# Kernel tuning notes

Measured on AMD Instinct MI355X. Metric: run time of the kernel, lower is better.

The kernel has to match this reference:

```python
import jax, jax.numpy as jnp
import numpy as np

NUM_LABELS = 10  # number of distinct label values in the minibatch
EPS = 1e-8


def setup_inputs() -> dict:
    key = jax.random.key(0)
    k1, k2 = jax.random.split(key)
    z = jax.random.normal(k1, (8192, 20, 256), dtype=jnp.float32)  # [B, C, H]
    labels = jax.random.randint(k2, (8192,), 0, NUM_LABELS)  # [B]
    return {"z": z, "labels": labels}


def reference(z, labels):
    # CODI minibatch loss, positive pairs, representation space.
    # Equivalent to: for each unique label, mse(z[group] + 1e-8, mean(z[group]))
    # summed over labels. Vectorized as a single segment-mean +
    # gather-broadcast + segment-SSE pass (one traversal of z).
    z = jnp.nan_to_num(z)
    B, C, H = z.shape
    counts = jax.ops.segment_sum(
        jnp.ones((B,), dtype=z.dtype), labels, num_segments=NUM_LABELS
    )  # [K]
    sums = jax.ops.segment_sum(z, labels, num_segments=NUM_LABELS)  # [K, C, H]
    means = jnp.nan_to_num(sums / jnp.maximum(counts, 1.0)[:, None, None])
    # per-sample squared distance to its group's mean (note the +EPS as in torch)
    d = (z + EPS) - means[labels]  # [B, C, H]
    per_sample = jnp.sum(d * d, axis=(1, 2))  # [B]
    sse = jax.ops.segment_sum(per_sample, labels, num_segments=NUM_LABELS)  # [K]
    # nn.MSELoss is a mean over all elements of the group: count_k * C * H
    mse_k = sse / (jnp.maximum(counts, 1.0) * (C * H))
    # torch.unique only visits labels present in the batch -> mask empty groups
    return jnp.sum(jnp.where(counts > 0, jnp.nan_to_num(mse_k), 0.0))
```

## Files before the change

### kernel.cpp

```cpp
#include <hip/hip_runtime.h>

#define B_SZ   8192
#define CH     5120
#define CH4    1280
#define K_LAB  10
#define EPS    1e-8f
#define FLTMAX 3.402823466e38f

#define RC_N   128
#define ROWS   64
#define CC_N   4
#define CCW    320
#define NT1    320

#define CG_N   20
#define NT2    64
#define RCSTRIDE (K_LAB * CC_N * CCW)


__device__ __forceinline__ float4 sanitize(float4 v) {
    v.x = (v.x == v.x) ? fminf(fmaxf(v.x, -FLTMAX), FLTMAX) : 0.f;
    v.y = (v.y == v.y) ? fminf(fmaxf(v.y, -FLTMAX), FLTMAX) : 0.f;
    v.z = (v.z == v.z) ? fminf(fmaxf(v.z, -FLTMAX), FLTMAX) : 0.f;
    v.w = (v.w == v.w) ? fminf(fmaxf(v.w, -FLTMAX), FLTMAX) : 0.f;
    return v;
}

__global__ __launch_bounds__(NT1) void codi_pass1(
    const float4* __restrict__ z4, const int* __restrict__ labels,
    float4* __restrict__ P_sum, float* __restrict__ P_ssq,
    int* __restrict__ P_cnt, int* __restrict__ done)
{
    const int tid = threadIdx.x;
    const int rc  = blockIdx.x >> 2;
    const int cc  = blockIdx.x & 3;

    __shared__ int   lab_s[ROWS];
    __shared__ float wssq[5][K_LAB];

    if (blockIdx.x == 0 && tid == 0) *done = 0;

    if (tid < ROWS) lab_s[tid] = labels[rc * ROWS + tid];
    __syncthreads();

    float4 sum[K_LAB];
    float  ssq[K_LAB];
    #pragma unroll
    for (int k = 0; k < K_LAB; ++k) {
        sum[k] = make_float4(0.f, 0.f, 0.f, 0.f);
        ssq[k] = 0.f;
    }

    const float4* zp = z4 + (size_t)rc * ROWS * CH4 + cc * CCW + tid;

    for (int r = 0; r < ROWS; r += 8) {
        float4 v[8];
        #pragma unroll
        for (int u = 0; u < 8; ++u) v[u] = zp[(size_t)(r + u) * CH4];

        #pragma unroll
        for (int u = 0; u < 8; ++u) {
            const int lab = __builtin_amdgcn_readfirstlane(lab_s[r + u]);
            float4 t = sanitize(v[u]);
            float  q = fmaf(t.x, t.x, fmaf(t.y, t.y, fmaf(t.z, t.z, t.w * t.w)));
            #pragma unroll
            for (int k = 0; k < K_LAB; ++k) {
                const float w = (lab == k) ? 1.f : 0.f;
                sum[k].x = fmaf(t.x, w, sum[k].x);
                sum[k].y = fmaf(t.y, w, sum[k].y);
                sum[k].z = fmaf(t.z, w, sum[k].z);
                sum[k].w = fmaf(t.w, w, sum[k].w);
                ssq[k]   = fmaf(q,   w, ssq[k]);
            }
        }
    }

    #pragma unroll
    for (int k = 0; k < K_LAB; ++k)
        P_sum[(((size_t)rc * K_LAB + k) * CC_N + cc) * CCW + tid] = sum[k];

    const int lane = tid & 63, wid = tid >> 6;
    #pragma unroll
    for (int k = 0; k < K_LAB; ++k) {
        float s = ssq[k];
        #pragma unroll
        for (int o = 32; o > 0; o >>= 1) s += __shfl_down(s, o, 64);
        if (lane == 0) wssq[wid][k] = s;
    }
    __syncthreads();
    if (tid < K_LAB) {
        float s = wssq[0][tid] + wssq[1][tid] + wssq[2][tid]
                + wssq[3][tid] + wssq[4][tid];
        P_ssq[(rc * CC_N + cc) * K_LAB + tid] = s;
    }

    if (cc == 0 && tid < 64) {
        const int lab = lab_s[tid];
        #pragma unroll
        for (int k = 0; k < K_LAB; ++k) {
            unsigned long long m = __ballot(lab == k);
            if (tid == k) P_cnt[rc * K_LAB + k] = __popcll(m);
        }
    }
}

__global__ __launch_bounds__(NT2) void codi_pass2(
    const float4* __restrict__ P_sum, const float* __restrict__ P_ssq,
    const int* __restrict__ P_cnt, float* __restrict__ pn,
    float* __restrict__ ssqk, float* __restrict__ cntk,
    int* __restrict__ done, float* __restrict__ out)
{
    const int tid = threadIdx.x;
    const int k   = blockIdx.x / CG_N;
    const int cg  = blockIdx.x % CG_N;
    const int c   = cg * NT2 + tid;
    const int cc  = c / CCW;
    const int co  = c % CCW;

    const float4* p = P_sum + ((size_t)k * CC_N + cc) * CCW + co;
    float4 s = make_float4(0.f, 0.f, 0.f, 0.f);
    #pragma unroll 16
    for (int rc = 0; rc < RC_N; ++rc) {
        float4 v = p[(size_t)rc * RCSTRIDE];
        s.x += v.x; s.y += v.y; s.z += v.z; s.w += v.w;
    }
    float q = fmaf(s.x, s.x, fmaf(s.y, s.y, fmaf(s.z, s.z, s.w * s.w)));
    #pragma unroll
    for (int o = 32; o > 0; o >>= 1) q += __shfl_down(q, o, 64);
    if (tid == 0) pn[k * CG_N + cg] = q;

    if (cg == 0) {
        float s2 = 0.f;
        for (int i = tid; i < RC_N * CC_N; i += NT2) s2 += P_ssq[i * K_LAB + k];
        #pragma unroll
        for (int o = 32; o > 0; o >>= 1) s2 += __shfl_down(s2, o, 64);
        int n = 0;
        for (int i = tid; i < RC_N; i += NT2) n += P_cnt[i * K_LAB + k];
        #pragma unroll
        for (int o = 32; o > 0; o >>= 1) n += __shfl_down(n, o, 64);
        if (tid == 0) { ssqk[k] = s2; cntk[k] = (float)n; }
    }

    __threadfence();
    __shared__ int ticket;
    if (tid == 0) ticket = atomicAdd(done, 1);
    __syncthreads();

    if (ticket == K_LAB * CG_N - 1) {
        float acc = 0.f;
        for (int k2 = 0; k2 < K_LAB; ++k2) {
            float np = 0.f;
            if (tid < CG_N) np = atomicAdd(&pn[k2 * CG_N + tid], 0.f);
            #pragma unroll
            for (int o = 32; o > 0; o >>= 1) np += __shfl_down(np, o, 64);
            if (tid == 0) {
                float nn = atomicAdd(&cntk[k2], 0.f);
                float s2 = atomicAdd(&ssqk[k2], 0.f);
                if (nn > 0.f) {
                    float sse = s2 - np / nn + nn * (float)CH * (EPS * EPS);
                    float mse = sse / (nn * (float)CH);
                    if (mse == mse) acc += mse;
                }
            }
        }
        if (tid == 0) out[0] = acc;
    }
}

extern "C" void kernel_launch(void* const* d_in, const int* in_sizes, int n_in,
                              void* d_out, int out_size, void* d_ws, size_t ws_size,
                              hipStream_t stream) {
    const float4* z4     = (const float4*)d_in[0];
    const int*    labels = (const int*)d_in[1];

    float*  hdr   = (float*)d_ws;
    int*    done  = (int*)hdr;
    float*  pn    = hdr + 16;
    float*  ssqk  = hdr + 224;
    float*  cntk  = hdr + 240;
    int*    P_cnt = (int*)(hdr + 256);
    float*  P_ssq = hdr + 1536;
    float4* P_sum = (float4*)(hdr + 6720);

    codi_pass1<<<RC_N * CC_N, NT1, 0, stream>>>(z4, labels, P_sum, P_ssq, P_cnt, done);
    codi_pass2<<<K_LAB * CG_N, NT2, 0, stream>>>(P_sum, P_ssq, P_cnt, pn, ssqk,
                                                 cntk, done, (float*)d_out);
}
```

Before: 272.6 us.

## Fuse two-pass CODI reduction into one kernel with last-block folding

Merges the partial-sum pass and the fold pass into one kernel. The last 40 blocks to finish, chosen by ticket, spin until every block has arrived, then each folds one (label, column-chunk) slice of the partial sums, and the final ticket holder computes the loss. This removes the second kernel launch and the dependency gap between launches. In exchange it adds a spin-wait whose correctness relies on all blocks being co-resident or scheduled, a memset launch to reset the counter, and a cap of 3 blocks per SIMD via launch bounds.

Measured after the change: 337.1 us. +23.7%, slower.

```diff
diff --git a/kernel.cpp b/kernel.cpp
--- a/kernel.cpp
+++ b/kernel.cpp
@@ -12,9 +12,8 @@
 #define CC_N   4
 #define CCW    320
 #define NT1    320
-
-#define CG_N   20
-#define NT2    64
+#define NBLK   (RC_N * CC_N)
+#define NFOLD  (K_LAB * CC_N)
 #define RCSTRIDE (K_LAB * CC_N * CCW)
 
 
@@ -26,19 +25,23 @@
     return v;
 }
 
-__global__ __launch_bounds__(NT1) void codi_pass1(
+__global__ __launch_bounds__(NT1, 3) void codi_fused(
     const float4* __restrict__ z4, const int* __restrict__ labels,
     float4* __restrict__ P_sum, float* __restrict__ P_ssq,
-    int* __restrict__ P_cnt, int* __restrict__ done)
+    int* __restrict__ P_cnt, float* __restrict__ pn,
+    float* __restrict__ ssqk, float* __restrict__ cntk,
+    int* __restrict__ done, float* __restrict__ out)
 {
-    const int tid = threadIdx.x;
-    const int rc  = blockIdx.x >> 2;
-    const int cc  = blockIdx.x & 3;
+    const int tid  = threadIdx.x;
+    const int lane = tid & 63, wid = tid >> 6;
+    const int rc   = blockIdx.x >> 2;
+    const int cc   = blockIdx.x & 3;
 
     __shared__ int   lab_s[ROWS];
     __shared__ float wssq[5][K_LAB];
-
-    if (blockIdx.x == 0 && tid == 0) *done = 0;
+    __shared__ float red_q[5], red_s[5];
+    __shared__ int   red_n[5];
+    __shared__ int   tkt;
 
     if (tid < ROWS) lab_s[tid] = labels[rc * ROWS + tid];
     __syncthreads();
@@ -52,7 +55,6 @@
     }
 
     const float4* zp = z4 + (size_t)rc * ROWS * CH4 + cc * CCW + tid;
-
     for (int r = 0; r < ROWS; r += 8) {
         float4 v[8];
         #pragma unroll
@@ -79,7 +81,6 @@
     for (int k = 0; k < K_LAB; ++k)
         P_sum[(((size_t)rc * K_LAB + k) * CC_N + cc) * CCW + tid] = sum[k];
 
-    const int lane = tid & 63, wid = tid >> 6;
     #pragma unroll
     for (int k = 0; k < K_LAB; ++k) {
         float s = ssq[k];
@@ -88,11 +89,9 @@
         if (lane == 0) wssq[wid][k] = s;
     }
     __syncthreads();
-    if (tid < K_LAB) {
-        float s = wssq[0][tid] + wssq[1][tid] + wssq[2][tid]
-                + wssq[3][tid] + wssq[4][tid];
-        P_ssq[(rc * CC_N + cc) * K_LAB + tid] = s;
-    }
+    if (tid < K_LAB)
+        P_ssq[(rc * CC_N + cc) * K_LAB + tid] =
+            wssq[0][tid] + wssq[1][tid] + wssq[2][tid] + wssq[3][tid] + wssq[4][tid];
 
     if (cc == 0 && tid < 64) {
         const int lab = lab_s[tid];
@@ -102,65 +101,72 @@
             if (tid == k) P_cnt[rc * K_LAB + k] = __popcll(m);
         }
     }
-}
 
-__global__ __launch_bounds__(NT2) void codi_pass2(
-    const float4* __restrict__ P_sum, const float* __restrict__ P_ssq,
-    const int* __restrict__ P_cnt, float* __restrict__ pn,
-    float* __restrict__ ssqk, float* __restrict__ cntk,
-    int* __restrict__ done, float* __restrict__ out)
-{
-    const int tid = threadIdx.x;
-    const int k   = blockIdx.x / CG_N;
-    const int cg  = blockIdx.x % CG_N;
-    const int c   = cg * NT2 + tid;
-    const int cc  = c / CCW;
-    const int co  = c % CCW;
+    __threadfence();
+    if (tid == 0) tkt = atomicAdd(done, 1);
+    __syncthreads();
+    const int t1 = tkt;
+    if (t1 < NBLK - NFOLD) return;
 
-    const float4* p = P_sum + ((size_t)k * CC_N + cc) * CCW + co;
-    float4 s = make_float4(0.f, 0.f, 0.f, 0.f);
+    if (tid == 0) {
+        while (__hip_atomic_load(done, __ATOMIC_RELAXED,
+                                 __HIP_MEMORY_SCOPE_AGENT) < NBLK)
+            __builtin_amdgcn_s_sleep(8);
+    }
+    __syncthreads();
+    __threadfence();
+
+    const int fid = t1 - (NBLK - NFOLD);
+    const int fk  = fid >> 2, fcc = fid & 3;
+
+    const float4* p = P_sum + ((size_t)fk * CC_N + fcc) * CCW + tid;
+    float4 s4 = make_float4(0.f, 0.f, 0.f, 0.f);
     #pragma unroll 16
-    for (int rc = 0; rc < RC_N; ++rc) {
-        float4 v = p[(size_t)rc * RCSTRIDE];
-        s.x += v.x; s.y += v.y; s.z += v.z; s.w += v.w;
+    for (int r2 = 0; r2 < RC_N; ++r2) {
+        float4 v = p[(size_t)r2 * RCSTRIDE];
+        s4.x += v.x; s4.y += v.y; s4.z += v.z; s4.w += v.w;
     }
-    float q = fmaf(s.x, s.x, fmaf(s.y, s.y, fmaf(s.z, s.z, s.w * s.w)));
+    float q = fmaf(s4.x, s4.x, fmaf(s4.y, s4.y, fmaf(s4.z, s4.z, s4.w * s4.w)));
     #pragma unroll
     for (int o = 32; o > 0; o >>= 1) q += __shfl_down(q, o, 64);
-    if (tid == 0) pn[k * CG_N + cg] = q;
 
-    if (cg == 0) {
-        float s2 = 0.f;
-        for (int i = tid; i < RC_N * CC_N; i += NT2) s2 += P_ssq[i * K_LAB + k];
-        #pragma unroll
-        for (int o = 32; o > 0; o >>= 1) s2 += __shfl_down(s2, o, 64);
-        int n = 0;
-        for (int i = tid; i < RC_N; i += NT2) n += P_cnt[i * K_LAB + k];
-        #pragma unroll
-        for (int o = 32; o > 0; o >>= 1) n += __shfl_down(n, o, 64);
-        if (tid == 0) { ssqk[k] = s2; cntk[k] = (float)n; }
+    float s2 = P_ssq[tid * K_LAB + fk]
+             + ((tid < 192) ? P_ssq[(tid + 320) * K_LAB + fk] : 0.f);
+    #pragma unroll
+    for (int o = 32; o > 0; o >>= 1) s2 += __shfl_down(s2, o, 64);
+    int n = (tid < RC_N) ? P_cnt[tid * K_LAB + fk] : 0;
+    #pragma unroll
+    for (int o = 32; o > 0; o >>= 1) n += __shfl_down(n, o, 64);
+
+    if (lane == 0) { red_q[wid] = q; red_s[wid] = s2; red_n[wid] = n; }
+    __syncthreads();
+    if (tid == 0) {
+        pn[fid] = red_q[0] + red_q[1] + red_q[2] + red_q[3] + red_q[4];
+        if (fcc == 0) {
+            ssqk[fk] = red_s[0] + red_s[1] + red_s[2] + red_s[3] + red_s[4];
+            cntk[fk] = (float)(red_n[0] + red_n[1] + red_n[2] + red_n[3] + red_n[4]);
+        }
     }
 
     __threadfence();
-    __shared__ int ticket;
-    if (tid == 0) ticket = atomicAdd(done, 1);
     __syncthreads();
-
-    if (ticket == K_LAB * CG_N - 1) {
+    if (tid == 0) tkt = atomicAdd(done, 1);
+    __syncthreads();
+    if (tkt == NBLK + NFOLD - 1 && tid < 64) {
+        float np4 = (tid < NFOLD) ? atomicAdd(&pn[tid], 0.f) : 0.f;
+        np4 += __shfl_down(np4, 2, 64);
+        np4 += __shfl_down(np4, 1, 64);
+        float s2v = (tid < K_LAB) ? atomicAdd(&ssqk[tid], 0.f) : 0.f;
+        float nnv = (tid < K_LAB) ? atomicAdd(&cntk[tid], 0.f) : 0.f;
         float acc = 0.f;
-        for (int k2 = 0; k2 < K_LAB; ++k2) {
-            float np = 0.f;
-            if (tid < CG_N) np = atomicAdd(&pn[k2 * CG_N + tid], 0.f);
-            #pragma unroll
-            for (int o = 32; o > 0; o >>= 1) np += __shfl_down(np, o, 64);
-            if (tid == 0) {
-                float nn = atomicAdd(&cntk[k2], 0.f);
-                float s2 = atomicAdd(&ssqk[k2], 0.f);
-                if (nn > 0.f) {
-                    float sse = s2 - np / nn + nn * (float)CH * (EPS * EPS);
-                    float mse = sse / (nn * (float)CH);
-                    if (mse == mse) acc += mse;
-                }
+        for (int k = 0; k < K_LAB; ++k) {
+            float np = __shfl(np4, 4 * k, 64);
+            float sk = __shfl(s2v, k, 64);
+            float nk = __shfl(nnv, k, 64);
+            if (nk > 0.f) {
+                float sse = sk - np / nk + nk * (float)CH * (EPS * EPS);
+                float mse = sse / (nk * (float)CH);
+                if (mse == mse) acc += mse;
             }
         }
         if (tid == 0) out[0] = acc;
@@ -176,13 +182,13 @@
     float*  hdr   = (float*)d_ws;
     int*    done  = (int*)hdr;
     float*  pn    = hdr + 16;
-    float*  ssqk  = hdr + 224;
-    float*  cntk  = hdr + 240;
-    int*    P_cnt = (int*)(hdr + 256);
+    float*  ssqk  = hdr + 64;
+    float*  cntk  = hdr + 80;
+    int*    P_cnt = (int*)(hdr + 96);
     float*  P_ssq = hdr + 1536;
     float4* P_sum = (float4*)(hdr + 6720);
 
-    codi_pass1<<<RC_N * CC_N, NT1, 0, stream>>>(z4, labels, P_sum, P_ssq, P_cnt, done);
-    codi_pass2<<<K_LAB * CG_N, NT2, 0, stream>>>(P_sum, P_ssq, P_cnt, pn, ssqk,
-                                                 cntk, done, (float*)d_out);
+    hipMemsetAsync(done, 0, sizeof(int), stream);
+    codi_fused<<<NBLK, NT1, 0, stream>>>(z4, labels, P_sum, P_ssq, P_cnt,
+                                         pn, ssqk, cntk, done, (float*)d_out);
 }
```
